# Performance work log

Hardware: AMD Instinct MI355X
Metric: run time of the kernel (lower is better)

The kernel has to match this reference:

```python
import jax, jax.numpy as jnp
import numpy as np

H = 768          # hidden_size
NH = 12          # num heads
HD = H // NH     # head dim = 64
FF = 4 * H       # 3072
EPS = 1e-12


def _layer_norm(x, g, b):
    mu = jnp.mean(x, axis=-1, keepdims=True)
    var = jnp.var(x, axis=-1, keepdims=True)
    return (x - mu) * jax.lax.rsqrt(var + EPS) * g + b


def setup_inputs() -> dict:
    key = jax.random.key(0)
    ks = jax.random.split(key, 8)
    B, S = 4, 2048
    s = 0.02
    return {
        "x": jax.random.normal(ks[0], (B, S, H), dtype=jnp.float32),
        "w_qkv": jax.random.normal(ks[1], (H, 3 * H), dtype=jnp.float32) * s,
        "b_qkv": jnp.zeros((3 * H,), dtype=jnp.float32),
        "w_out": jax.random.normal(ks[2], (H, H), dtype=jnp.float32) * s,
        "b_out": jnp.zeros((H,), dtype=jnp.float32),
        "w_ff1": jax.random.normal(ks[3], (H, FF), dtype=jnp.float32) * s,
        "b_ff1": jnp.zeros((FF,), dtype=jnp.float32),
        "w_ff2": jax.random.normal(ks[4], (FF, H), dtype=jnp.float32) * s,
        "b_ff2": jnp.zeros((H,), dtype=jnp.float32),
        "g1": jnp.ones((H,), dtype=jnp.float32),
        "be1": jnp.zeros((H,), dtype=jnp.float32),
        "g2": jnp.ones((H,), dtype=jnp.float32),
        "be2": jnp.zeros((H,), dtype=jnp.float32),
    }


def reference(x, w_qkv, b_qkv, w_out, b_out, w_ff1, b_ff1, w_ff2, b_ff2, g1, be1, g2, be2):
    B, S, _ = x.shape
    qkv = x @ w_qkv + b_qkv                     # [B,S,3H]
    q, k, v = jnp.split(qkv, 3, axis=-1)
    # [B,S,H] -> [B,NH,S,HD]
    def heads(t):
        return t.reshape(B, S, NH, HD).transpose(0, 2, 1, 3)
    q, k, v = heads(q), heads(k), heads(v)
    scores = jnp.einsum("bhqd,bhkd->bhqk", q, k) / np.sqrt(HD).astype(np.float32)
    attn = jax.nn.softmax(scores, axis=-1)      # dropout is identity at inference
    ctx = jnp.einsum("bhqk,bhkd->bhqd", attn, v)
    ctx = ctx.transpose(0, 2, 1, 3).reshape(B, S, H)
    attn_out = ctx @ w_out + b_out
    x1 = _layer_norm(x + attn_out, g1, be1)
    h = jax.nn.gelu(x1 @ w_ff1 + b_ff1, approximate=False)  # torch exact gelu
    ffn = h @ w_ff2 + b_ff2
    return _layer_norm(x1 + ffn, g2, be2)
```

## Files before the change

### kernel.cpp

```cpp
#include <hip/hip_runtime.h>
#include <cstdint>
#include <cstddef>

typedef unsigned short u16;
typedef __attribute__((ext_vector_type(8))) short bf16x8;
typedef __attribute__((ext_vector_type(4))) float f32x4;
typedef __attribute__((ext_vector_type(16))) float f32x16;

__device__ __forceinline__ u16 f2b(float f) {
    union { float f; unsigned u; } un; un.f = f;
    unsigned r = un.u + 0x7fffu + ((un.u >> 16) & 1u);
    return (u16)(r >> 16);
}
__device__ __forceinline__ u16 f2b_trunc(float f) {
    union { float f; unsigned u; } un; un.f = f;
    return (u16)(un.u >> 16);
}
__device__ __forceinline__ float b2f(u16 h) {
    union { unsigned u; float f; } un; un.u = ((unsigned)h) << 16;
    return un.f;
}
__device__ __forceinline__ float fast_exp2(float x) {
#if __has_builtin(__builtin_amdgcn_exp2f)
    return __builtin_amdgcn_exp2f(x);
#else
    return exp2f(x);
#endif
}
__device__ __forceinline__ float fast_rcp(float x) {
#if __has_builtin(__builtin_amdgcn_rcpf)
    return __builtin_amdgcn_rcpf(x);
#else
    return 1.f / x;
#endif
}
__device__ __forceinline__ float gelu_fast(float v) {
    const float s = fast_exp2(v * (2.30220842f + 0.10294324f * (v * v)));
    return v - v * fast_rcp(s + 1.f);
}

__device__ __forceinline__ void stage16(const u16* g, u16* l) {
    __builtin_amdgcn_global_load_lds(
        (const __attribute__((address_space(1))) void*)g,
        (__attribute__((address_space(3))) void*)l, 16, 0, 0);
}

__global__ __launch_bounds__(256)
void prep(const float* __restrict__ x, u16* __restrict__ xb,
          const float* __restrict__ wqkv, u16* __restrict__ wqkvT,
          const float* __restrict__ wout, u16* __restrict__ woutT,
          const float* __restrict__ wff1, u16* __restrict__ wff1T,
          const float* __restrict__ wff2, u16* __restrict__ wff2T) {
    __shared__ float t[32][33];
    const int tid = threadIdx.x;
    int bid = blockIdx.x;
    if (bid < 6144) {
        const int i = bid * 256 + tid;
        float4 v = ((const float4*)x)[i];
        ushort4 o;
        o.x = f2b(v.x); o.y = f2b(v.y); o.z = f2b(v.z); o.w = f2b(v.w);
        ((ushort4*)xb)[i] = o;
        return;
    }
    int tt = bid - 6144;
    const float* in; u16* out; int K, N, bx, by;
    if (tt < 1728)      { in = wqkv; out = wqkvT; K = 768;  N = 2304; bx = tt % 72; by = tt / 72; }
    else if ((tt -= 1728) < 576)  { in = wout; out = woutT; K = 768;  N = 768;  bx = tt % 24; by = tt / 24; }
    else if ((tt -= 576) < 2304)  { in = wff1; out = wff1T; K = 768;  N = 3072; bx = tt % 96; by = tt / 96; }
    else { tt -= 2304;    in = wff2; out = wff2T; K = 3072; N = 768;  bx = tt % 24; by = tt / 24; }
    const int n0 = bx * 32, k0 = by * 32;
    const int tx = tid & 31, ty = tid >> 5;
#pragma unroll
    for (int i = 0; i < 4; ++i)
        t[ty + i * 8][tx] = in[(size_t)(k0 + ty + i * 8) * N + n0 + tx];
    __syncthreads();
#pragma unroll
    for (int i = 0; i < 4; ++i)
        out[(size_t)(n0 + ty + i * 8) * K + k0 + tx] = f2b(t[tx][ty + i * 8]);
}

template <int EPI, int NTW>
__global__ __launch_bounds__(256, 3)
void gemm_bf16(const u16* __restrict__ A, const u16* __restrict__ BT,
               const float* __restrict__ bias,
               void* __restrict__ outp, u16* __restrict__ vt, int M, int N, int K) {
    __shared__ __align__(16) u16 Ash[128 * 64];
    __shared__ __align__(16) u16 Bsh[NTW * 64 * 64];
    const int m0 = blockIdx.y * 128, n0 = blockIdx.x * (NTW * 64);
    const int tid = threadIdx.x;
    const int w = tid >> 6, lane = tid & 63;
    const int l32 = lane & 31, half = lane >> 5;
    const int wm = (w >> 1) * 64, wn = (w & 1) * (NTW * 32);

    const int srow = lane >> 3;
    const int sgrp = (lane & 7) ^ (srow & 7);
    const int xr = l32 & 7;

    f32x16 acc[2][NTW];
#pragma unroll
    for (int i = 0; i < 2; ++i)
#pragma unroll
        for (int j = 0; j < NTW; ++j)
#pragma unroll
            for (int e = 0; e < 16; ++e) acc[i][j][e] = 0.f;

    for (int k0 = 0; k0 < K; k0 += 64) {
#pragma unroll
        for (int it = 0; it < 4; ++it) {
            const int c = it * 4 + w;
            const int r = c * 8 + srow;
            stage16(A + (size_t)(m0 + r) * K + k0 + sgrp * 8, &Ash[c * 512 + lane * 8]);
        }
#pragma unroll
        for (int it = 0; it < 2 * NTW; ++it) {
            const int c = it * 4 + w;
            const int r = c * 8 + srow;
            stage16(BT + (size_t)(n0 + r) * K + k0 + sgrp * 8, &Bsh[c * 512 + lane * 8]);
        }
        __syncthreads();

        if constexpr (NTW == 2) {
            bf16x8 af[2][4], bfr[2][4];
#pragma unroll
            for (int mt = 0; mt < 2; ++mt)
#pragma unroll
                for (int kc = 0; kc < 4; ++kc)
                    af[mt][kc] = *(const bf16x8*)&Ash[(wm + mt * 32 + l32) * 64 +
                                                      (((kc << 1) + half) ^ xr) * 8];
#pragma unroll
            for (int nt = 0; nt < 2; ++nt)
#pragma unroll
                for (int kc = 0; kc < 4; ++kc)
                    bfr[nt][kc] = *(const bf16x8*)&Bsh[(wn + nt * 32 + l32) * 64 +
                                                       (((kc << 1) + half) ^ xr) * 8];
#pragma unroll
            for (int mt = 0; mt < 2; ++mt)
#pragma unroll
                for (int nt = 0; nt < 2; ++nt)
#pragma unroll
                    for (int kc = 0; kc < 4; ++kc)
                        acc[mt][nt] = __builtin_amdgcn_mfma_f32_32x32x16_bf16(
                            af[mt][kc], bfr[nt][kc], acc[mt][nt], 0, 0, 0);
        } else {
#pragma unroll
            for (int kc = 0; kc < 4; ++kc) {
                const int ko = (((kc << 1) + half) ^ xr) * 8;
                bf16x8 a0 = *(const bf16x8*)&Ash[(wm + l32) * 64 + ko];
                bf16x8 a1 = *(const bf16x8*)&Ash[(wm + 32 + l32) * 64 + ko];
#pragma unroll
                for (int nt = 0; nt < NTW; ++nt) {
                    bf16x8 bv = *(const bf16x8*)&Bsh[(wn + nt * 32 + l32) * 64 + ko];
                    acc[0][nt] = __builtin_amdgcn_mfma_f32_32x32x16_bf16(
                        a0, bv, acc[0][nt], 0, 0, 0);
                    acc[1][nt] = __builtin_amdgcn_mfma_f32_32x32x16_bf16(
                        a1, bv, acc[1][nt], 0, 0, 0);
                }
            }
        }
        __syncthreads();
    }

    if (EPI == 3 && n0 >= 1536) {
#pragma unroll
        for (int mt = 0; mt < 2; ++mt) {
#pragma unroll
            for (int nt = 0; nt < NTW; ++nt) {
                const int col = n0 + wn + nt * 32 + l32;
                const int c = col - 1536;
                const int h = c >> 6, d = c & 63;
                const float bv = bias[col];
#pragma unroll
                for (int rq = 0; rq < 4; ++rq) {
                    const int row0 = m0 + wm + mt * 32 + rq * 8 + half * 4;
                    const int b = row0 >> 11, tok = row0 & 2047;
                    ushort4 o;
                    o.x = f2b(acc[mt][nt][rq * 4 + 0] + bv);
                    o.y = f2b(acc[mt][nt][rq * 4 + 1] + bv);
                    o.z = f2b(acc[mt][nt][rq * 4 + 2] + bv);
                    o.w = f2b(acc[mt][nt][rq * 4 + 3] + bv);
                    *(ushort4*)&vt[(size_t)(((b * 12 + h) << 6) + d) * 2048 + tok] = o;
                }
            }
        }
        return;
    }

#pragma unroll
    for (int mt = 0; mt < 2; ++mt) {
#pragma unroll
        for (int nt = 0; nt < NTW; ++nt) {
            const int col = n0 + wn + nt * 32 + l32;
            const float bv = bias[col];
#pragma unroll
            for (int reg = 0; reg < 16; ++reg) {
                const int row = m0 + wm + mt * 32 + (reg & 3) + 8 * (reg >> 2) + 4 * half;
                float v = acc[mt][nt][reg] + bv;
                if (EPI == 2)
                    v = gelu_fast(v);
                ((u16*)outp)[(size_t)row * N + col] = f2b(v);
            }
        }
    }
}

template <bool RESF32>
__global__ __launch_bounds__(256, 4)
void gemm_bf16_r64(const u16* __restrict__ A, const u16* __restrict__ BT,
                   const float* __restrict__ bias, const void* __restrict__ resid,
                   u16* __restrict__ outp, int M, int N, int K) {
    __shared__ __align__(16) u16 Ash[64 * 64];
    __shared__ __align__(16) u16 Bsh[128 * 64];
    const int m0 = blockIdx.y * 64, n0 = blockIdx.x * 128;
    const int tid = threadIdx.x;
    const int w = tid >> 6, lane = tid & 63;
    const int l32 = lane & 31, half = lane >> 5;
    const int wm = (w >> 1) * 32, wn = (w & 1) * 64;

    const int srow = lane >> 3;
    const int sgrp = (lane & 7) ^ (srow & 7);
    const int xr = l32 & 7;

    f32x16 acc[2];
#pragma unroll
    for (int j = 0; j < 2; ++j)
#pragma unroll
        for (int e = 0; e < 16; ++e) acc[j][e] = 0.f;

    for (int k0 = 0; k0 < K; k0 += 64) {
#pragma unroll
        for (int it = 0; it < 2; ++it) {
            const int c = it * 4 + w;
            const int r = c * 8 + srow;
            stage16(A + (size_t)(m0 + r) * K + k0 + sgrp * 8, &Ash[c * 512 + lane * 8]);
        }
#pragma unroll
        for (int it = 0; it < 4; ++it) {
            const int c = it * 4 + w;
            const int r = c * 8 + srow;
            stage16(BT + (size_t)(n0 + r) * K + k0 + sgrp * 8, &Bsh[c * 512 + lane * 8]);
        }
        __syncthreads();

        bf16x8 af[4], bfr[2][4];
#pragma unroll
        for (int kc = 0; kc < 4; ++kc)
            af[kc] = *(const bf16x8*)&Ash[(wm + l32) * 64 + (((kc << 1) + half) ^ xr) * 8];
#pragma unroll
        for (int nt = 0; nt < 2; ++nt)
#pragma unroll
            for (int kc = 0; kc < 4; ++kc)
                bfr[nt][kc] = *(const bf16x8*)&Bsh[(wn + nt * 32 + l32) * 64 +
                                                   (((kc << 1) + half) ^ xr) * 8];
#pragma unroll
        for (int nt = 0; nt < 2; ++nt)
#pragma unroll
            for (int kc = 0; kc < 4; ++kc)
                acc[nt] = __builtin_amdgcn_mfma_f32_32x32x16_bf16(
                    af[kc], bfr[nt][kc], acc[nt], 0, 0, 0);
        __syncthreads();
    }

#pragma unroll
    for (int nt = 0; nt < 2; ++nt) {
        const int col = n0 + wn + nt * 32 + l32;
        const float bv = bias[col];
#pragma unroll
        for (int reg = 0; reg < 16; ++reg) {
            const int row = m0 + wm + (reg & 3) + 8 * (reg >> 2) + 4 * half;
            const size_t idx = (size_t)row * N + col;
            const float rv = RESF32 ? ((const float*)resid)[idx]
                                    : b2f(((const u16*)resid)[idx]);
            outp[idx] = f2b(acc[nt][reg] + bv + rv);
        }
    }
}

__global__ __launch_bounds__(256, 3)
void attn_fused(const u16* __restrict__ qkv, const u16* __restrict__ vt,
                u16* __restrict__ ctx) {
    constexpr int LDP = 68;
    __shared__ __align__(16) u16 Ksh[64 * 64];
    __shared__ __align__(16) u16 Vsh[64 * 64];
    __shared__ __align__(16) short Psh[4 * 32 * LDP];

    const int q0 = blockIdx.x * 128;
    const int h = blockIdx.y, b = blockIdx.z;
    const int tid = threadIdx.x;
    const int w = tid >> 6, lane = tid & 63, l16 = lane & 15, quad = lane >> 4;
    short* Pw = Psh + w * 32 * LDP;

    const int srow = lane >> 3;
    const int sgrp = (lane & 7) ^ (srow & 7);
    const int xk = l16 & 7;

    const u16* Qp = qkv + (size_t)b * 2048 * 2304 + h * 64;
    const u16* Kp = Qp + 768;
    const u16* Vtp = vt + ((size_t)(b * 12 + h) << 6) * 2048;

    bf16x8 qf[2][2];
#pragma unroll
    for (int mt = 0; mt < 2; ++mt)
#pragma unroll
        for (int s = 0; s < 2; ++s)
            qf[mt][s] = *(const bf16x8*)(Qp +
                (size_t)(q0 + w * 32 + mt * 16 + l16) * 2304 + s * 32 + quad * 8);

    const f32x4 vzero = {0.f, 0.f, 0.f, 0.f};
    f32x4 oacc[2][4];
    float l_r[2][4];
#pragma unroll
    for (int mt = 0; mt < 2; ++mt) {
#pragma unroll
        for (int dt = 0; dt < 4; ++dt) oacc[mt][dt] = vzero;
#pragma unroll
        for (int r = 0; r < 4; ++r) l_r[mt][r] = 0.f;
    }

    constexpr float SCALE = 0.18033688011112042f;

    for (int kt = 0; kt < 2048; kt += 64) {
#pragma unroll
        for (int it = 0; it < 2; ++it) {
            const int c = it * 4 + w;
            const int r = c * 8 + srow;
            stage16(Kp + (size_t)(kt + r) * 2304 + sgrp * 8, &Ksh[c * 512 + lane * 8]);
        }
#pragma unroll
        for (int it = 0; it < 2; ++it) {
            const int c = it * 4 + w;
            const int r = c * 8 + srow;
            stage16(Vtp + (size_t)r * 2048 + kt + sgrp * 8, &Vsh[c * 512 + lane * 8]);
        }
        __syncthreads();

        bf16x8 kfr[4][2];
#pragma unroll
        for (int nt = 0; nt < 4; ++nt)
#pragma unroll
            for (int s = 0; s < 2; ++s)
                kfr[nt][s] = *(const bf16x8*)&Ksh[(nt * 16 + l16) * 64 +
                                                  (((s << 2) + quad) ^ xk) * 8];

        f32x4 sacc[2][4];
#pragma unroll
        for (int mt = 0; mt < 2; ++mt)
#pragma unroll
            for (int nt = 0; nt < 4; ++nt) {
                sacc[mt][nt] = vzero;
#pragma unroll
                for (int s = 0; s < 2; ++s)
                    sacc[mt][nt] = __builtin_amdgcn_mfma_f32_16x16x32_bf16(
                        qf[mt][s], kfr[nt][s], sacc[mt][nt], 0, 0, 0);
            }

#pragma unroll
        for (int mt = 0; mt < 2; ++mt) {
#pragma unroll
            for (int r = 0; r < 4; ++r) {
                float p0 = fast_exp2(sacc[mt][0][r] * SCALE);
                float p1 = fast_exp2(sacc[mt][1][r] * SCALE);
                float p2 = fast_exp2(sacc[mt][2][r] * SCALE);
                float p3 = fast_exp2(sacc[mt][3][r] * SCALE);
                l_r[mt][r] += (p0 + p1) + (p2 + p3);
                short* prow = &Pw[(mt * 16 + quad * 4 + r) * LDP + l16];
                prow[0]  = (short)f2b_trunc(p0);
                prow[16] = (short)f2b_trunc(p1);
                prow[32] = (short)f2b_trunc(p2);
                prow[48] = (short)f2b_trunc(p3);
            }
        }

        bf16x8 vfr[4][2];
#pragma unroll
        for (int dt = 0; dt < 4; ++dt)
#pragma unroll
            for (int s = 0; s < 2; ++s)
                vfr[dt][s] = *(const bf16x8*)&Vsh[(dt * 16 + l16) * 64 +
                                                  (((s << 2) + quad) ^ xk) * 8];

#pragma unroll
        for (int mt = 0; mt < 2; ++mt) {
            bf16x8 pf[2];
#pragma unroll
            for (int s = 0; s < 2; ++s) {
                union { struct { short4 lo, hi; } h2; bf16x8 v; } u;
                const short* base = &Pw[(mt * 16 + l16) * LDP + s * 32 + quad * 8];
                u.h2.lo = *(const short4*)(base);
                u.h2.hi = *(const short4*)(base + 4);
                pf[s] = u.v;
            }
#pragma unroll
            for (int dt = 0; dt < 4; ++dt)
#pragma unroll
                for (int s = 0; s < 2; ++s)
                    oacc[mt][dt] = __builtin_amdgcn_mfma_f32_16x16x32_bf16(
                        pf[s], vfr[dt][s], oacc[mt][dt], 0, 0, 0);
        }
        __syncthreads();
    }

#pragma unroll
    for (int mt = 0; mt < 2; ++mt)
#pragma unroll
        for (int r = 0; r < 4; ++r) {
#pragma unroll
            for (int off = 1; off < 16; off <<= 1)
                l_r[mt][r] += __shfl_xor(l_r[mt][r], off);
            l_r[mt][r] = 1.f / l_r[mt][r];
        }

#pragma unroll
    for (int mt = 0; mt < 2; ++mt)
#pragma unroll
        for (int dt = 0; dt < 4; ++dt)
#pragma unroll
            for (int r = 0; r < 4; ++r) {
                const int row = q0 + w * 32 + mt * 16 + quad * 4 + r;
                ctx[(size_t)(b * 2048 + row) * 768 + h * 64 + dt * 16 + l16] =
                    f2b(oacc[mt][dt][r] * l_r[mt][r]);
            }
}

template <bool OUTF32>
__global__ __launch_bounds__(256)
void layernorm_k(const u16* __restrict__ y, const float* __restrict__ g,
                 const float* __restrict__ be, float* __restrict__ outf,
                 u16* __restrict__ outb) {
    const int row = blockIdx.x;
    const int tid = threadIdx.x;
    const u16* yr = y + (size_t)row * 768;
    float v[3], s = 0.f, s2 = 0.f;
#pragma unroll
    for (int i = 0; i < 3; ++i) {
        float x = b2f(yr[tid + i * 256]);
        v[i] = x; s += x; s2 += x * x;
    }
#pragma unroll
    for (int off = 32; off >= 1; off >>= 1) {
        s += __shfl_xor(s, off);
        s2 += __shfl_xor(s2, off);
    }
    __shared__ float red[2][4];
    const int w = tid >> 6;
    if ((tid & 63) == 0) { red[0][w] = s; red[1][w] = s2; }
    __syncthreads();
    s = red[0][0] + red[0][1] + red[0][2] + red[0][3];
    s2 = red[1][0] + red[1][1] + red[1][2] + red[1][3];
    const float mu = s * (1.f / 768.f);
    const float var = s2 * (1.f / 768.f) - mu * mu;
    const float rs = rsqrtf(var + 1e-12f);
#pragma unroll
    for (int i = 0; i < 3; ++i) {
        const int c = tid + i * 256;
        const float o = (v[i] - mu) * rs * g[c] + be[c];
        if (OUTF32) outf[(size_t)row * 768 + c] = o;
        else        outb[(size_t)row * 768 + c] = f2b(o);
    }
}

extern "C" void kernel_launch(void* const* d_in, const int* in_sizes, int n_in,
                              void* d_out, int out_size, void* d_ws, size_t ws_size,
                              hipStream_t stream) {
    const float* x    = (const float*)d_in[0];
    const float* wqkv = (const float*)d_in[1];
    const float* bqkv = (const float*)d_in[2];
    const float* wout = (const float*)d_in[3];
    const float* bout = (const float*)d_in[4];
    const float* wff1 = (const float*)d_in[5];
    const float* bff1 = (const float*)d_in[6];
    const float* wff2 = (const float*)d_in[7];
    const float* bff2 = (const float*)d_in[8];
    const float* g1   = (const float*)d_in[9];
    const float* be1  = (const float*)d_in[10];
    const float* g2   = (const float*)d_in[11];
    const float* be2  = (const float*)d_in[12];

    char* ws = (char*)d_ws;
    constexpr size_t o_xb    = 0;
    constexpr size_t o_wqkvT = o_xb    + (size_t)8192 * 768 * 2;
    constexpr size_t o_woutT = o_wqkvT + (size_t)2304 * 768 * 2;
    constexpr size_t o_wff1T = o_woutT + (size_t)768 * 768 * 2;
    constexpr size_t o_wff2T = o_wff1T + (size_t)3072 * 768 * 2;
    constexpr size_t o_qkv   = o_wff2T + (size_t)768 * 3072 * 2;
    constexpr size_t o_ctx   = o_qkv   + (size_t)8192 * 2304 * 2;
    constexpr size_t o_y     = o_ctx   + (size_t)8192 * 768 * 2;
    constexpr size_t o_x1b   = o_y     + (size_t)8192 * 768 * 2;
    constexpr size_t o_vt    = o_x1b;
    constexpr size_t o_h     = o_qkv;

    u16*   xb    = (u16*)(ws + o_xb);
    u16*   wqkvT = (u16*)(ws + o_wqkvT);
    u16*   woutT = (u16*)(ws + o_woutT);
    u16*   wff1T = (u16*)(ws + o_wff1T);
    u16*   wff2T = (u16*)(ws + o_wff2T);
    u16*   qkvb  = (u16*)(ws + o_qkv);
    u16*   ctxb  = (u16*)(ws + o_ctx);
    u16*   yb    = (u16*)(ws + o_y);
    u16*   x1b   = (u16*)(ws + o_x1b);
    u16*   hb    = (u16*)(ws + o_h);
    u16*   vt    = (u16*)(ws + o_vt);

    prep<<<13056, 256, 0, stream>>>(x, xb, wqkv, wqkvT, wout, woutT,
                                    wff1, wff1T, wff2, wff2T);

    gemm_bf16<3, 3><<<dim3(2304 / 192, 8192 / 128), 256, 0, stream>>>(
        xb, wqkvT, bqkv, qkvb, vt, 8192, 2304, 768);

    attn_fused<<<dim3(2048 / 128, 12, 4), 256, 0, stream>>>(qkvb, vt, ctxb);

    gemm_bf16_r64<true><<<dim3(768 / 128, 8192 / 64), 256, 0, stream>>>(
        ctxb, woutT, bout, x, yb, 8192, 768, 768);

    layernorm_k<false><<<8192, 256, 0, stream>>>(yb, g1, be1, nullptr, x1b);

    gemm_bf16<2, 2><<<dim3(3072 / 128, 8192 / 128), 256, 0, stream>>>(
        x1b, wff1T, bff1, hb, nullptr, 8192, 3072, 768);

    gemm_bf16_r64<false><<<dim3(768 / 128, 8192 / 64), 256, 0, stream>>>(
        hb, wff2T, bff2, x1b, yb, 8192, 768, 3072);

    layernorm_k<true><<<8192, 256, 0, stream>>>(yb, g2, be2, (float*)d_out, nullptr);
}
```

Measured before the change: 387.8 us.

## Double-buffer K/V tiles in attention and swizzle block order across XCDs

The attention kernel now double-buffers its K and V shared-memory tiles. It issues the next tile's global-to-LDS loads before computing on the current one, using explicit vmcnt waits and raw barriers instead of __syncthreads. The grid becomes 1D with a block-index swizzle, so blocks sharing a (batch, head) land on the same XCD for L2 reuse, and s_setprio raises wave priority around the MFMA sections. This doubles K/V LDS use, which may lower occupancy under launch_bounds(256,3), and relies on the stage16 load count matching vmcnt(4).

```diff
diff --git a/kernel.cpp b/kernel.cpp
--- a/kernel.cpp
+++ b/kernel.cpp
@@ -279,12 +279,16 @@
 void attn_fused(const u16* __restrict__ qkv, const u16* __restrict__ vt,
                 u16* __restrict__ ctx) {
     constexpr int LDP = 68;
-    __shared__ __align__(16) u16 Ksh[64 * 64];
-    __shared__ __align__(16) u16 Vsh[64 * 64];
+    __shared__ __align__(16) u16 Ksh[2][64 * 64];
+    __shared__ __align__(16) u16 Vsh[2][64 * 64];
     __shared__ __align__(16) short Psh[4 * 32 * LDP];
 
-    const int q0 = blockIdx.x * 128;
-    const int h = blockIdx.y, b = blockIdx.z;
+    const int orig = blockIdx.x;
+    const int swz = (orig & 7) * 96 + (orig >> 3);
+    const int q0 = (swz & 15) * 128;
+    const int bh = swz >> 4;
+    const int h = bh % 12, b = bh / 12;
+
     const int tid = threadIdx.x;
     const int w = tid >> 6, lane = tid & 63, l16 = lane & 15, quad = lane >> 4;
     short* Pw = Psh + w * 32 * LDP;
@@ -304,6 +308,8 @@
         for (int s = 0; s < 2; ++s)
             qf[mt][s] = *(const bf16x8*)(Qp +
                 (size_t)(q0 + w * 32 + mt * 16 + l16) * 2304 + s * 32 + quad * 8);
+    asm volatile("s_waitcnt vmcnt(0)" ::: "memory");
+    __builtin_amdgcn_sched_barrier(0);
 
     const f32x4 vzero = {0.f, 0.f, 0.f, 0.f};
     f32x4 oacc[2][4];
@@ -318,30 +324,46 @@
 
     constexpr float SCALE = 0.18033688011112042f;
 
-    for (int kt = 0; kt < 2048; kt += 64) {
+    auto stage_kv = [&](int buf, int ktt) {
 #pragma unroll
         for (int it = 0; it < 2; ++it) {
             const int c = it * 4 + w;
             const int r = c * 8 + srow;
-            stage16(Kp + (size_t)(kt + r) * 2304 + sgrp * 8, &Ksh[c * 512 + lane * 8]);
+            stage16(Kp + (size_t)(ktt + r) * 2304 + sgrp * 8,
+                    &Ksh[buf][c * 512 + lane * 8]);
         }
 #pragma unroll
         for (int it = 0; it < 2; ++it) {
             const int c = it * 4 + w;
             const int r = c * 8 + srow;
-            stage16(Vtp + (size_t)r * 2048 + kt + sgrp * 8, &Vsh[c * 512 + lane * 8]);
-        }
-        __syncthreads();
+            stage16(Vtp + (size_t)r * 2048 + ktt + sgrp * 8,
+                    &Vsh[buf][c * 512 + lane * 8]);
+        }
+    };
+
+    stage_kv(0, 0);
+
+    for (int t = 0; t < 32; ++t) {
+        const int cur = t & 1;
+        if (t < 31) {
+            stage_kv(cur ^ 1, (t + 1) * 64);
+            asm volatile("s_waitcnt vmcnt(4)" ::: "memory");
+        } else {
+            asm volatile("s_waitcnt vmcnt(0)" ::: "memory");
+        }
+        __builtin_amdgcn_sched_barrier(0);
+        __builtin_amdgcn_s_barrier();
 
         bf16x8 kfr[4][2];
 #pragma unroll
         for (int nt = 0; nt < 4; ++nt)
 #pragma unroll
             for (int s = 0; s < 2; ++s)
-                kfr[nt][s] = *(const bf16x8*)&Ksh[(nt * 16 + l16) * 64 +
-                                                  (((s << 2) + quad) ^ xk) * 8];
+                kfr[nt][s] = *(const bf16x8*)&Ksh[cur][(nt * 16 + l16) * 64 +
+                                                      (((s << 2) + quad) ^ xk) * 8];
 
         f32x4 sacc[2][4];
+        __builtin_amdgcn_s_setprio(1);
 #pragma unroll
         for (int mt = 0; mt < 2; ++mt)
 #pragma unroll
@@ -352,6 +374,7 @@
                     sacc[mt][nt] = __builtin_amdgcn_mfma_f32_16x16x32_bf16(
                         qf[mt][s], kfr[nt][s], sacc[mt][nt], 0, 0, 0);
             }
+        __builtin_amdgcn_s_setprio(0);
 
 #pragma unroll
         for (int mt = 0; mt < 2; ++mt) {
@@ -375,9 +398,10 @@
         for (int dt = 0; dt < 4; ++dt)
 #pragma unroll
             for (int s = 0; s < 2; ++s)
-                vfr[dt][s] = *(const bf16x8*)&Vsh[(dt * 16 + l16) * 64 +
-                                                  (((s << 2) + quad) ^ xk) * 8];
-
+                vfr[dt][s] = *(const bf16x8*)&Vsh[cur][(dt * 16 + l16) * 64 +
+                                                      (((s << 2) + quad) ^ xk) * 8];
+
+        __builtin_amdgcn_s_setprio(1);
 #pragma unroll
         for (int mt = 0; mt < 2; ++mt) {
             bf16x8 pf[2];
@@ -396,7 +420,8 @@
                     oacc[mt][dt] = __builtin_amdgcn_mfma_f32_16x16x32_bf16(
                         pf[s], vfr[dt][s], oacc[mt][dt], 0, 0, 0);
         }
-        __syncthreads();
+        __builtin_amdgcn_s_setprio(0);
+        __builtin_amdgcn_s_barrier();
     }
 
 #pragma unroll
@@ -506,7 +531,7 @@
     gemm_bf16<3, 3><<<dim3(2304 / 192, 8192 / 128), 256, 0, stream>>>(
         xb, wqkvT, bqkv, qkvb, vt, 8192, 2304, 768);
 
-    attn_fused<<<dim3(2048 / 128, 12, 4), 256, 0, stream>>>(qkvb, vt, ctxb);
+    attn_fused<<<768, 256, 0, stream>>>(qkvb, vt, ctxb);
 
     gemm_bf16_r64<true><<<dim3(768 / 128, 8192 / 64), 256, 0, stream>>>(
         ctxb, woutT, bout, x, yb, 8192, 768, 768);
```

Result: no change. 385.9 us (-0.5%).
